# Optimization experiments

Measured on AMD Instinct MI355X. Metric: run time of the kernel, lower is better.

Reference implementation:

```python
import jax, jax.numpy as jnp
import numpy as np

B, L, HID = 4, 4096, 1024
H, D = 16, 64  # num_heads, head_dim


def setup_inputs() -> dict:
    key = jax.random.key(0)
    ks = jax.random.split(key, 5)
    s = 1.0 / np.sqrt(HID)
    mk = lambda k: jax.random.uniform(k, (HID, HID), minval=-s, maxval=s, dtype=jnp.float32)
    return {
        "x": jax.random.normal(ks[0], (B, L, HID), dtype=jnp.float32),
        "Wq": mk(ks[1]), "bq": jnp.zeros((HID,), jnp.float32),
        "Wk": mk(ks[2]), "bk": jnp.zeros((HID,), jnp.float32),
        "Wv": mk(ks[3]), "bv": jnp.zeros((HID,), jnp.float32),
        "Wo": mk(ks[4]), "bo": jnp.zeros((HID,), jnp.float32),
    }


def reference(x, Wq, bq, Wk, bk, Wv, bv, Wo, bo):
    Bx, Lx, _ = x.shape
    # projections (weights stored [in, out])
    q = (x @ Wq + bq).reshape(Bx, Lx, H, D)
    k = (x @ Wk + bk).reshape(Bx, Lx, H, D)
    v = (x @ Wv + bv).reshape(Bx, Lx, H, D)
    # Single window (L <= window_size): torch matmul batches over (B, L) and
    # contracts head_dim -> per-token head-to-head scores [B, L, H, H].
    scores = jnp.einsum('blhd,bled->blhe', q, k) / np.sqrt(D).astype(np.float32)
    probs = jax.nn.softmax(scores, axis=-1)
    out = jnp.einsum('blhe,bled->blhd', probs, v).reshape(Bx, Lx, HID)
    return out @ Wo + bo
```

## Files before the change

### kernel.cpp

```cpp
#include <hip/hip_runtime.h>
#include <stdint.h>


typedef __attribute__((ext_vector_type(8))) short short8;
typedef __attribute__((ext_vector_type(4))) float floatx4;
typedef __attribute__((address_space(1))) unsigned int gu32;
typedef __attribute__((address_space(3))) unsigned int lu32;

#define HID 1024
#define MTOK 16384
#define WELEM (HID * HID)
#define XELEM (MTOK * HID)

__device__ __forceinline__ unsigned short f2bf(float f) {
  union { float f; uint32_t u; } v; v.f = f;
  uint32_t u = v.u;
  u += 0x7fffu + ((u >> 16) & 1u);
  return (unsigned short)(u >> 16);
}

__global__ __launch_bounds__(256) void cvt_x_kernel(const float* __restrict__ x,
                                                    unsigned short* __restrict__ xb) {
  const int idx = blockIdx.x * 256 + threadIdx.x;
  float4 v = ((const float4*)x)[idx];
  ushort4 o;
  o.x = f2bf(v.x); o.y = f2bf(v.y); o.z = f2bf(v.z); o.w = f2bf(v.w);
  ((ushort4*)xb)[idx] = o;
}

__global__ __launch_bounds__(256) void cvt_w_kernel(const float* __restrict__ W0,
                                                    const float* __restrict__ W1,
                                                    const float* __restrict__ W2,
                                                    const float* __restrict__ W3,
                                                    unsigned short* __restrict__ WT) {
  const float* W = (blockIdx.z == 0) ? W0 : (blockIdx.z == 1) ? W1
                   : (blockIdx.z == 2) ? W2 : W3;
  unsigned short* out = WT + (size_t)blockIdx.z * WELEM;
  __shared__ float tile[64][65];
  const int t = threadIdx.x;
  const int n0 = blockIdx.x * 64, k0 = blockIdx.y * 64;
#pragma unroll
  for (int i = 0; i < 4; i++) {
    const int row = i * 16 + (t >> 4);
    const int col = (t & 15) * 4;
    float4 v = *(const float4*)&W[(size_t)(k0 + row) * HID + n0 + col];
    tile[row][col] = v.x; tile[row][col + 1] = v.y;
    tile[row][col + 2] = v.z; tile[row][col + 3] = v.w;
  }
  __syncthreads();
#pragma unroll
  for (int i = 0; i < 4; i++) {
    const int n = i * 16 + (t >> 4);
    const int k = (t & 15) * 4;
    ushort4 o;
    o.x = f2bf(tile[k][n]);     o.y = f2bf(tile[k + 1][n]);
    o.z = f2bf(tile[k + 2][n]); o.w = f2bf(tile[k + 3][n]);
    *(ushort4*)&out[(size_t)(n0 + n) * HID + k0 + k] = o;
  }
}

template <bool QKV>
__global__ __launch_bounds__(256) void gemm_bt1d(
    const unsigned short* __restrict__ A,
    const unsigned short* __restrict__ BTb,
    const float* __restrict__ b0, const float* __restrict__ b1,
    const float* __restrict__ b2,
    void* __restrict__ Cv)
{
  const int i = blockIdx.x;
  const int xcd = i & 7;
  const int j = i >> 3;
  int mb, nb;
  if constexpr (QKV) {
    const int round = j / 192;
    const int jj = j - round * 192;
    nb = jj >> 3;
    mb = xcd * 8 + round * 64 + (jj & 7);
  } else {
    const int round = j >> 5;
    const int jj = j & 31;
    nb = jj >> 2;
    mb = xcd * 4 + round * 32 + (jj & 3);
  }
  const int z = QKV ? (nb >> 3) : 0;
  const int n0 = QKV ? ((nb & 7) * 128) : (nb * 128);
  const int m0 = mb * 128;
  const unsigned short* BT = BTb + (size_t)(QKV ? z : 3) * WELEM;
  const float* bias = QKV ? ((z == 0) ? b0 : ((z == 1) ? b1 : b2)) : b0;

  __shared__ unsigned short Als[128 * 32];
  __shared__ unsigned short Bls[128 * 32];

  const int t = threadIdx.x;
  const int wv = t >> 6;
  const int lane = t & 63;
  const int quad = lane >> 4;
  const int r16 = lane & 15;
  const int wr = wv >> 1, wc = wv & 1;

  floatx4 acc[4][4] = {};

  const int srow = t >> 2;
  const int scol = (t & 3) * 8;
  const unsigned short* Ag = A + (size_t)(m0 + srow) * HID + scol;
  const unsigned short* Bg = BT + (size_t)(n0 + srow) * HID + scol;
  unsigned short* Asl = Als + (wv * 16) * 32;
  unsigned short* Bsl = Bls + (wv * 16) * 32;

  for (int ko = 0; ko < HID; ko += 32) {
    __builtin_amdgcn_global_load_lds((const gu32*)(Ag + ko),            (lu32*)(Asl),            16, 0, 0);
    __builtin_amdgcn_global_load_lds((const gu32*)(Ag + 64 * HID + ko), (lu32*)(Asl + 64 * 32),  16, 0, 0);
    __builtin_amdgcn_global_load_lds((const gu32*)(Bg + ko),            (lu32*)(Bsl),            16, 0, 0);
    __builtin_amdgcn_global_load_lds((const gu32*)(Bg + 64 * HID + ko), (lu32*)(Bsl + 64 * 32),  16, 0, 0);
    __syncthreads();

    short8 a[4], b[4];
#pragma unroll
    for (int ii = 0; ii < 4; ii++)
      a[ii] = *(const short8*)(Als + (wr * 64 + ii * 16 + r16) * 32 + quad * 8);
#pragma unroll
    for (int jj = 0; jj < 4; jj++)
      b[jj] = *(const short8*)(Bls + (wc * 64 + jj * 16 + r16) * 32 + quad * 8);
#pragma unroll
    for (int ii = 0; ii < 4; ii++)
#pragma unroll
      for (int jj = 0; jj < 4; jj++)
        acc[ii][jj] = __builtin_amdgcn_mfma_f32_16x16x32_bf16(a[ii], b[jj], acc[ii][jj], 0, 0, 0);
    __syncthreads();
  }

#pragma unroll
  for (int jj = 0; jj < 4; jj++) {
    const int col = n0 + wc * 64 + jj * 16 + r16;
    const float bb = bias[col];
#pragma unroll
    for (int ii = 0; ii < 4; ii++) {
      const int row0 = m0 + wr * 64 + ii * 16 + quad * 4;
#pragma unroll
      for (int rr = 0; rr < 4; rr++) {
        const float val = acc[ii][jj][rr] + bb;
        if constexpr (QKV)
          ((unsigned short*)Cv)[(size_t)z * XELEM + (size_t)(row0 + rr) * HID + col] = f2bf(val);
        else
          ((float*)Cv)[(size_t)(row0 + rr) * HID + col] = val;
      }
    }
  }
}

__global__ __launch_bounds__(256) void attn_kernel(const unsigned short* qkv,
                                                   unsigned short* attn) {
  __shared__ unsigned short vls[4][1056];
  __shared__ unsigned short pls[4][16 * 24];

  const int t = threadIdx.x;
  const int wv = t >> 6, lane = t & 63;
  const int quad = lane >> 4, r16 = lane & 15;
  const size_t base = ((size_t)blockIdx.x * 4 + wv) * HID;
  const unsigned short* qp = qkv + base;
  const unsigned short* kp = qkv + (size_t)XELEM + base;
  const unsigned short* vp = qkv + 2 * (size_t)XELEM + base;

  __builtin_amdgcn_global_load_lds((const gu32*)(vp + lane * 8),       (lu32*)&vls[wv][0],   16, 0, 0);
  __builtin_amdgcn_global_load_lds((const gu32*)(vp + 512 + lane * 8), (lu32*)&vls[wv][528], 16, 0, 0);

  short8 qf0 = *(const short8*)(qp + r16 * 64 + quad * 8);
  short8 qf1 = *(const short8*)(qp + r16 * 64 + quad * 8 + 32);
  short8 kf0 = *(const short8*)(kp + r16 * 64 + quad * 8);
  short8 kf1 = *(const short8*)(kp + r16 * 64 + quad * 8 + 32);

  floatx4 sc = {0.f, 0.f, 0.f, 0.f};
  sc = __builtin_amdgcn_mfma_f32_16x16x32_bf16(qf0, kf0, sc, 0, 0, 0);
  sc = __builtin_amdgcn_mfma_f32_16x16x32_bf16(qf1, kf1, sc, 0, 0, 0);

#pragma unroll
  for (int rr = 0; rr < 4; rr++) {
    float s = sc[rr] * 0.125f;
    float m = s;
#pragma unroll
    for (int off = 1; off < 16; off <<= 1) m = fmaxf(m, __shfl_xor(m, off));
    float ex = __expf(s - m);
    float sum = ex;
#pragma unroll
    for (int off = 1; off < 16; off <<= 1) sum += __shfl_xor(sum, off);
    pls[wv][(quad * 4 + rr) * 24 + r16] = f2bf(ex / sum);
  }

  __syncthreads();

  const short8 zero8 = {0, 0, 0, 0, 0, 0, 0, 0};
  short8 af = zero8;
  short8 bf[4] = {zero8, zero8, zero8, zero8};
  if (quad < 2) {
    af = *(const short8*)&pls[wv][r16 * 24 + quad * 8];
#pragma unroll
    for (int c = 0; c < 4; c++)
#pragma unroll
      for (int jj = 0; jj < 8; jj++)
        bf[c][jj] = (short)vls[wv][quad * 528 + jj * 64 + c * 16 + r16];
  }

  floatx4 ov[4];
#pragma unroll
  for (int c = 0; c < 4; c++) {
    floatx4 z = {0.f, 0.f, 0.f, 0.f};
    ov[c] = __builtin_amdgcn_mfma_f32_16x16x32_bf16(af, bf[c], z, 0, 0, 0);
  }

#pragma unroll
  for (int rr = 0; rr < 4; rr++)
#pragma unroll
    for (int c = 0; c < 4; c++)
      attn[base + (size_t)(quad * 4 + rr) * 64 + c * 16 + r16] = f2bf(ov[c][rr]);
}

extern "C" void kernel_launch(void* const* d_in, const int* in_sizes, int n_in,
                              void* d_out, int out_size, void* d_ws, size_t ws_size,
                              hipStream_t stream) {
  const float* x  = (const float*)d_in[0];
  const float* Wq = (const float*)d_in[1];
  const float* bq = (const float*)d_in[2];
  const float* Wk = (const float*)d_in[3];
  const float* bk = (const float*)d_in[4];
  const float* Wv = (const float*)d_in[5];
  const float* bv = (const float*)d_in[6];
  const float* Wo = (const float*)d_in[7];
  const float* bo = (const float*)d_in[8];

  char* ws = (char*)d_ws;
  unsigned short* xb  = (unsigned short*)ws;
  unsigned short* wt  = (unsigned short*)(ws + (size_t)XELEM * 2);
  unsigned short* qkv = wt + 4 * (size_t)WELEM;

  cvt_x_kernel<<<XELEM / 1024, 256, 0, stream>>>(x, xb);
  cvt_w_kernel<<<dim3(16, 16, 4), 256, 0, stream>>>(Wq, Wk, Wv, Wo, wt);
  gemm_bt1d<true><<<3072, 256, 0, stream>>>(xb, wt, bq, bk, bv, (void*)qkv);
  attn_kernel<<<4096, 256, 0, stream>>>(qkv, qkv);
  gemm_bt1d<false><<<1024, 256, 0, stream>>>(qkv, wt, bo, bo, bo, d_out);
}
```

Before: 333.0 us.

## Deepen GEMM K-step to 64 via two LDS stages and split QKV launch

The GEMM main loop now loads two 32-wide K slices into separate LDS buffers per iteration and computes both before the next barrier. This halves the number of barriers and batches more global loads in flight. The QKV projection is also split into two launches of half the M rows each, with the tile-index mapping simplified to match. The cost is doubled LDS per block, which may lower occupancy, plus one extra launch.

```diff
diff --git a/kernel.cpp b/kernel.cpp
--- a/kernel.cpp
+++ b/kernel.cpp
@@ -65,17 +65,15 @@
     const unsigned short* __restrict__ BTb,
     const float* __restrict__ b0, const float* __restrict__ b1,
     const float* __restrict__ b2,
-    void* __restrict__ Cv)
+    void* __restrict__ Cv, int mbase)
 {
   const int i = blockIdx.x;
   const int xcd = i & 7;
   const int j = i >> 3;
   int mb, nb;
   if constexpr (QKV) {
-    const int round = j / 192;
-    const int jj = j - round * 192;
-    nb = jj >> 3;
-    mb = xcd * 8 + round * 64 + (jj & 7);
+    nb = j >> 3;
+    mb = mbase + xcd * 8 + (j & 7);
   } else {
     const int round = j >> 5;
     const int jj = j & 31;
@@ -88,8 +86,8 @@
   const unsigned short* BT = BTb + (size_t)(QKV ? z : 3) * WELEM;
   const float* bias = QKV ? ((z == 0) ? b0 : ((z == 1) ? b1 : b2)) : b0;
 
-  __shared__ unsigned short Als[128 * 32];
-  __shared__ unsigned short Bls[128 * 32];
+  __shared__ unsigned short Als[2][128 * 32];
+  __shared__ unsigned short Bls[2][128 * 32];
 
   const int t = threadIdx.x;
   const int wv = t >> 6;
@@ -104,28 +102,34 @@
   const int scol = (t & 3) * 8;
   const unsigned short* Ag = A + (size_t)(m0 + srow) * HID + scol;
   const unsigned short* Bg = BT + (size_t)(n0 + srow) * HID + scol;
-  unsigned short* Asl = Als + (wv * 16) * 32;
-  unsigned short* Bsl = Bls + (wv * 16) * 32;
-
-  for (int ko = 0; ko < HID; ko += 32) {
-    __builtin_amdgcn_global_load_lds((const gu32*)(Ag + ko),            (lu32*)(Asl),            16, 0, 0);
-    __builtin_amdgcn_global_load_lds((const gu32*)(Ag + 64 * HID + ko), (lu32*)(Asl + 64 * 32),  16, 0, 0);
-    __builtin_amdgcn_global_load_lds((const gu32*)(Bg + ko),            (lu32*)(Bsl),            16, 0, 0);
-    __builtin_amdgcn_global_load_lds((const gu32*)(Bg + 64 * HID + ko), (lu32*)(Bsl + 64 * 32),  16, 0, 0);
+  const int wbase = (wv * 16) * 32;
+
+  for (int ko = 0; ko < HID; ko += 64) {
+#pragma unroll
+    for (int s = 0; s < 2; s++) {
+      const int kk = ko + s * 32;
+      __builtin_amdgcn_global_load_lds((const gu32*)(Ag + kk),            (lu32*)(Als[s] + wbase),           16, 0, 0);
+      __builtin_amdgcn_global_load_lds((const gu32*)(Ag + 64 * HID + kk), (lu32*)(Als[s] + wbase + 64 * 32), 16, 0, 0);
+      __builtin_amdgcn_global_load_lds((const gu32*)(Bg + kk),            (lu32*)(Bls[s] + wbase),           16, 0, 0);
+      __builtin_amdgcn_global_load_lds((const gu32*)(Bg + 64 * HID + kk), (lu32*)(Bls[s] + wbase + 64 * 32), 16, 0, 0);
+    }
     __syncthreads();
 
-    short8 a[4], b[4];
-#pragma unroll
-    for (int ii = 0; ii < 4; ii++)
-      a[ii] = *(const short8*)(Als + (wr * 64 + ii * 16 + r16) * 32 + quad * 8);
-#pragma unroll
-    for (int jj = 0; jj < 4; jj++)
-      b[jj] = *(const short8*)(Bls + (wc * 64 + jj * 16 + r16) * 32 + quad * 8);
-#pragma unroll
-    for (int ii = 0; ii < 4; ii++)
+#pragma unroll
+    for (int s = 0; s < 2; s++) {
+      short8 a[4], b[4];
+#pragma unroll
+      for (int ii = 0; ii < 4; ii++)
+        a[ii] = *(const short8*)(Als[s] + (wr * 64 + ii * 16 + r16) * 32 + quad * 8);
 #pragma unroll
       for (int jj = 0; jj < 4; jj++)
-        acc[ii][jj] = __builtin_amdgcn_mfma_f32_16x16x32_bf16(a[ii], b[jj], acc[ii][jj], 0, 0, 0);
+        b[jj] = *(const short8*)(Bls[s] + (wc * 64 + jj * 16 + r16) * 32 + quad * 8);
+#pragma unroll
+      for (int ii = 0; ii < 4; ii++)
+#pragma unroll
+        for (int jj = 0; jj < 4; jj++)
+          acc[ii][jj] = __builtin_amdgcn_mfma_f32_16x16x32_bf16(a[ii], b[jj], acc[ii][jj], 0, 0, 0);
+    }
     __syncthreads();
   }
 
@@ -234,7 +238,8 @@
 
   cvt_x_kernel<<<XELEM / 1024, 256, 0, stream>>>(x, xb);
   cvt_w_kernel<<<dim3(16, 16, 4), 256, 0, stream>>>(Wq, Wk, Wv, Wo, wt);
-  gemm_bt1d<true><<<3072, 256, 0, stream>>>(xb, wt, bq, bk, bv, (void*)qkv);
+  gemm_bt1d<true><<<1536, 256, 0, stream>>>(xb, wt, bq, bk, bv, (void*)qkv, 0);
+  gemm_bt1d<true><<<1536, 256, 0, stream>>>(xb, wt, bq, bk, bv, (void*)qkv, 64);
   attn_kernel<<<4096, 256, 0, stream>>>(qkv, qkv);
-  gemm_bt1d<false><<<1024, 256, 0, stream>>>(qkv, wt, bo, bo, bo, d_out);
-}
+  gemm_bt1d<false><<<1024, 256, 0, stream>>>(qkv, wt, bo, bo, bo, d_out, 0);
+}
```

New measurement: 350.2 us. 5.2% more time.

## Use 32x32x16 MFMA with XOR-swizzled LDS and merge conversion kernels

Applied to the files above, without the earlier changes.

Switches the projection GEMM inner loop from 16x16x32 MFMA tiles to 32x32x16 tiles, so each wave issues fewer, larger matrix ops with fewer LDS fragment reads. The LDS layout is XOR-swizzled by row to avoid bank conflicts on the wider fragment reads, and the epilogue is remapped to the 32x32 accumulator layout. The x and weight bf16 conversion kernels are merged into one launch to save a kernel launch. The main risk is a mistake in the swizzle or accumulator row mapping, which would give wrong results.

```diff
diff --git a/kernel.cpp b/kernel.cpp
--- a/kernel.cpp
+++ b/kernel.cpp
@@ -4,6 +4,7 @@
 
 typedef __attribute__((ext_vector_type(8))) short short8;
 typedef __attribute__((ext_vector_type(4))) float floatx4;
+typedef __attribute__((ext_vector_type(16))) float floatx16;
 typedef __attribute__((address_space(1))) unsigned int gu32;
 typedef __attribute__((address_space(3))) unsigned int lu32;
 
@@ -19,26 +20,27 @@
   return (unsigned short)(u >> 16);
 }
 
-__global__ __launch_bounds__(256) void cvt_x_kernel(const float* __restrict__ x,
-                                                    unsigned short* __restrict__ xb) {
-  const int idx = blockIdx.x * 256 + threadIdx.x;
-  float4 v = ((const float4*)x)[idx];
-  ushort4 o;
-  o.x = f2bf(v.x); o.y = f2bf(v.y); o.z = f2bf(v.z); o.w = f2bf(v.w);
-  ((ushort4*)xb)[idx] = o;
-}
-
-__global__ __launch_bounds__(256) void cvt_w_kernel(const float* __restrict__ W0,
-                                                    const float* __restrict__ W1,
-                                                    const float* __restrict__ W2,
-                                                    const float* __restrict__ W3,
-                                                    unsigned short* __restrict__ WT) {
-  const float* W = (blockIdx.z == 0) ? W0 : (blockIdx.z == 1) ? W1
-                   : (blockIdx.z == 2) ? W2 : W3;
-  unsigned short* out = WT + (size_t)blockIdx.z * WELEM;
+__global__ __launch_bounds__(256) void cvt_all_kernel(
+    const float* __restrict__ x, const float* __restrict__ W0,
+    const float* __restrict__ W1, const float* __restrict__ W2,
+    const float* __restrict__ W3, unsigned short* __restrict__ xb,
+    unsigned short* __restrict__ WT) {
+  const int t = threadIdx.x;
+  int bid = blockIdx.x;
+  if (bid < 16384) {
+    const int idx = bid * 256 + t;
+    float4 v = ((const float4*)x)[idx];
+    ushort4 o;
+    o.x = f2bf(v.x); o.y = f2bf(v.y); o.z = f2bf(v.z); o.w = f2bf(v.w);
+    ((ushort4*)xb)[idx] = o;
+    return;
+  }
+  bid -= 16384;
+  const int zz = bid >> 8, r = bid & 255;
+  const float* W = (zz == 0) ? W0 : (zz == 1) ? W1 : (zz == 2) ? W2 : W3;
+  unsigned short* out = WT + (size_t)zz * WELEM;
   __shared__ float tile[64][65];
-  const int t = threadIdx.x;
-  const int n0 = blockIdx.x * 64, k0 = blockIdx.y * 64;
+  const int n0 = (r & 15) * 64, k0 = (r >> 4) * 64;
 #pragma unroll
   for (int i = 0; i < 4; i++) {
     const int row = i * 16 + (t >> 4);
@@ -94,55 +96,60 @@
   const int t = threadIdx.x;
   const int wv = t >> 6;
   const int lane = t & 63;
-  const int quad = lane >> 4;
-  const int r16 = lane & 15;
+  const int l31 = lane & 31;
+  const int lh = lane >> 5;
   const int wr = wv >> 1, wc = wv & 1;
 
-  floatx4 acc[4][4] = {};
+  floatx16 acc[2][2] = {};
 
   const int srow = t >> 2;
-  const int scol = (t & 3) * 8;
-  const unsigned short* Ag = A + (size_t)(m0 + srow) * HID + scol;
-  const unsigned short* Bg = BT + (size_t)(n0 + srow) * HID + scol;
-  unsigned short* Asl = Als + (wv * 16) * 32;
-  unsigned short* Bsl = Bls + (wv * 16) * 32;
+  const int sch = (t & 3) ^ (srow & 3);
+  const unsigned short* Ag = A + (size_t)(m0 + srow) * HID + sch * 8;
+  const unsigned short* Bg = BT + (size_t)(n0 + srow) * HID + sch * 8;
+  const int wbase = (wv * 16) * 32;
 
   for (int ko = 0; ko < HID; ko += 32) {
-    __builtin_amdgcn_global_load_lds((const gu32*)(Ag + ko),            (lu32*)(Asl),            16, 0, 0);
-    __builtin_amdgcn_global_load_lds((const gu32*)(Ag + 64 * HID + ko), (lu32*)(Asl + 64 * 32),  16, 0, 0);
-    __builtin_amdgcn_global_load_lds((const gu32*)(Bg + ko),            (lu32*)(Bsl),            16, 0, 0);
-    __builtin_amdgcn_global_load_lds((const gu32*)(Bg + 64 * HID + ko), (lu32*)(Bsl + 64 * 32),  16, 0, 0);
+    __builtin_amdgcn_global_load_lds((const gu32*)(Ag + ko),            (lu32*)(Als + wbase),           16, 0, 0);
+    __builtin_amdgcn_global_load_lds((const gu32*)(Ag + 64 * HID + ko), (lu32*)(Als + wbase + 64 * 32), 16, 0, 0);
+    __builtin_amdgcn_global_load_lds((const gu32*)(Bg + ko),            (lu32*)(Bls + wbase),           16, 0, 0);
+    __builtin_amdgcn_global_load_lds((const gu32*)(Bg + 64 * HID + ko), (lu32*)(Bls + wbase + 64 * 32), 16, 0, 0);
     __syncthreads();
 
-    short8 a[4], b[4];
-#pragma unroll
-    for (int ii = 0; ii < 4; ii++)
-      a[ii] = *(const short8*)(Als + (wr * 64 + ii * 16 + r16) * 32 + quad * 8);
-#pragma unroll
-    for (int jj = 0; jj < 4; jj++)
-      b[jj] = *(const short8*)(Bls + (wc * 64 + jj * 16 + r16) * 32 + quad * 8);
-#pragma unroll
-    for (int ii = 0; ii < 4; ii++)
-#pragma unroll
-      for (int jj = 0; jj < 4; jj++)
-        acc[ii][jj] = __builtin_amdgcn_mfma_f32_16x16x32_bf16(a[ii], b[jj], acc[ii][jj], 0, 0, 0);
+    short8 a[2][2], b[2][2];
+#pragma unroll
+    for (int ti = 0; ti < 2; ti++)
+#pragma unroll
+      for (int kh = 0; kh < 2; kh++) {
+        const int ra = wr * 64 + ti * 32 + l31;
+        a[ti][kh] = *(const short8*)(Als + ra * 32 + (((lh + 2 * kh) ^ (ra & 3)) * 8));
+        const int rb = wc * 64 + ti * 32 + l31;
+        b[ti][kh] = *(const short8*)(Bls + rb * 32 + (((lh + 2 * kh) ^ (rb & 3)) * 8));
+      }
+#pragma unroll
+    for (int kh = 0; kh < 2; kh++)
+#pragma unroll
+      for (int ti = 0; ti < 2; ti++)
+#pragma unroll
+        for (int tj = 0; tj < 2; tj++)
+          acc[ti][tj] = __builtin_amdgcn_mfma_f32_32x32x16_bf16(a[ti][kh], b[tj][kh], acc[ti][tj], 0, 0, 0);
     __syncthreads();
   }
 
 #pragma unroll
-  for (int jj = 0; jj < 4; jj++) {
-    const int col = n0 + wc * 64 + jj * 16 + r16;
+  for (int tj = 0; tj < 2; tj++) {
+    const int col = n0 + wc * 64 + tj * 32 + l31;
     const float bb = bias[col];
 #pragma unroll
-    for (int ii = 0; ii < 4; ii++) {
-      const int row0 = m0 + wr * 64 + ii * 16 + quad * 4;
-#pragma unroll
-      for (int rr = 0; rr < 4; rr++) {
-        const float val = acc[ii][jj][rr] + bb;
+    for (int ti = 0; ti < 2; ti++) {
+      const int rbase = m0 + wr * 64 + ti * 32 + 4 * lh;
+#pragma unroll
+      for (int reg = 0; reg < 16; reg++) {
+        const int row = rbase + (reg & 3) + 8 * (reg >> 2);
+        const float val = acc[ti][tj][reg] + bb;
         if constexpr (QKV)
-          ((unsigned short*)Cv)[(size_t)z * XELEM + (size_t)(row0 + rr) * HID + col] = f2bf(val);
+          ((unsigned short*)Cv)[(size_t)z * XELEM + (size_t)row * HID + col] = f2bf(val);
         else
-          ((float*)Cv)[(size_t)(row0 + rr) * HID + col] = val;
+          ((float*)Cv)[(size_t)row * HID + col] = val;
       }
     }
   }
@@ -203,8 +210,8 @@
   floatx4 ov[4];
 #pragma unroll
   for (int c = 0; c < 4; c++) {
-    floatx4 z = {0.f, 0.f, 0.f, 0.f};
-    ov[c] = __builtin_amdgcn_mfma_f32_16x16x32_bf16(af, bf[c], z, 0, 0, 0);
+    floatx4 zz = {0.f, 0.f, 0.f, 0.f};
+    ov[c] = __builtin_amdgcn_mfma_f32_16x16x32_bf16(af, bf[c], zz, 0, 0, 0);
   }
 
 #pragma unroll
@@ -232,8 +239,7 @@
   unsigned short* wt  = (unsigned short*)(ws + (size_t)XELEM * 2);
   unsigned short* qkv = wt + 4 * (size_t)WELEM;
 
-  cvt_x_kernel<<<XELEM / 1024, 256, 0, stream>>>(x, xb);
-  cvt_w_kernel<<<dim3(16, 16, 4), 256, 0, stream>>>(Wq, Wk, Wv, Wo, wt);
+  cvt_all_kernel<<<16384 + 1024, 256, 0, stream>>>(x, Wq, Wk, Wv, Wo, xb, wt);
   gemm_bt1d<true><<<3072, 256, 0, stream>>>(xb, wt, bq, bk, bv, (void*)qkv);
   attn_kernel<<<4096, 256, 0, stream>>>(qkv, qkv);
   gemm_bt1d<false><<<1024, 256, 0, stream>>>(qkv, wt, bo, bo, bo, d_out);
```

Measured after the change: 365.2 us. +9.7%, slower.
